# Kernel optimization log

Measured on AMD Instinct MI355X. Metric: run time of the kernel, lower is better.

The kernel has to match this reference:

```python
import jax, jax.numpy as jnp
import numpy as np

# ---- CRF hyperparameters (init_kwargs) ----
NUM_CLASSES = 4
RADIUS = 10            # guided filter radius -> 21x21 kernel
EPS = 1e-4
THETA_GAMMA = 2.5
G_RADIUS = int(THETA_GAMMA * 4)  # gaussian layer radius = 10 -> 21x21 kernel
SPATIAL_COMPAT = 3.0
BILATERAL_COMPAT = 10.0
NUM_ITERATIONS = 5
RGB_W = np.array([0.2989, 0.5870, 0.1140], dtype=np.float32)  # tf rgb_to_grayscale


def _make_kernel(radius, theta):
    x, y = np.mgrid[-radius:radius + 1, -radius:radius + 1]
    k = np.exp(-(x ** 2 + y ** 2) / (2.0 * theta ** 2))
    k = k / k.sum()
    k[radius, radius] = 0.0  # zero out center (no self-message)
    return jnp.asarray(k, dtype=jnp.float32)

_GAUSS_K = _make_kernel(G_RADIUS, THETA_GAMMA)          # spatial gaussian kernel
_GUIDED_K = _make_kernel(RADIUS, RADIUS / 3.0)          # guided-filter gaussian kernel


def _depthwise(src, k2d, r):
    # src: [B,H,W,C], k2d: [kh,kw]; zero-padded depthwise conv (same as pad+VALID)
    c = src.shape[-1]
    kh, kw = k2d.shape
    k = jnp.broadcast_to(k2d[:, :, None, None], (kh, kw, 1, c))
    return jax.lax.conv_general_dilated(
        src, k, window_strides=(1, 1), padding=[(r, r), (r, r)],
        dimension_numbers=('NHWC', 'HWIO', 'NHWC'), feature_group_count=c)


def _gaussian(src):
    return _depthwise(src, _GAUSS_K, G_RADIUS)


def _guided(gray, p):
    # guided gaussian filter with single-channel guide `gray` [B,H,W,1]
    gf = lambda s: _depthwise(s, _GUIDED_K, RADIUS)
    mean_I = gf(gray)                       # [B,H,W,1]
    mean_p = gf(p)                          # [B,H,W,C]
    mean_Ip = gf(gray * p)
    cov_Ip = mean_Ip - mean_I * mean_p
    mean_II = gf(gray * gray)
    var_I = mean_II - mean_I * mean_I
    a = cov_Ip / (var_I + EPS)
    b = mean_p - a * mean_I
    return gf(a) * gray + gf(b)


def setup_inputs() -> dict:
    key = jax.random.key(0)
    k1, k2 = jax.random.split(key)
    unary = jax.random.normal(k1, (1, 512, 512, NUM_CLASSES), dtype=jnp.float32)
    image = jax.random.uniform(k2, (1, 512, 512, 3), dtype=jnp.float32)
    return {"unary": unary, "image": image}


def reference(unary, image):
    gray = (image @ jnp.asarray(RGB_W))[..., None]        # [B,H,W,1]
    ones = jnp.ones_like(unary)
    spatial_norm = _gaussian(ones)
    bilateral_norm = _guided(gray, ones)

    Q = jax.nn.softmax(-unary, axis=-1)
    for _ in range(NUM_ITERATIONS):
        spatial_out = _gaussian(Q) / spatial_norm
        bilateral_out = _guided(gray, Q) / bilateral_norm
        # spatial_weights = SPATIAL_COMPAT*I, bilateral_weights = BILATERAL_COMPAT*I,
        # compatibility = -I  => matmuls reduce to scalar scaling + negation
        message = SPATIAL_COMPAT * spatial_out + BILATERAL_COMPAT * bilateral_out
        pairwise = -message
        Q = jax.nn.softmax(-unary - pairwise, axis=-1)
    return Q
```

## Files before the change

kernel.cpp:

```cpp
#include <hip/hip_runtime.h>
#include <hip/hip_cooperative_groups.h>
#include <hip/hip_fp16.h>
#include <math.h>

namespace cg = cooperative_groups;

#define W 512
#define H 512
#define NPIX (W*H)
#define RAD 10
#define KS 21
#define CRF_EPS 1e-4f

#define TX 32
#define TY 8
#define CIN (TX + 2*RAD)
#define RIN (TY + 2*RAD)
#define GX (W / TX)
#define GY (H / TY)
#define NBLK (GX*GY)
#define NVT (CIN * 4)

#define SM_BYTES 30784
#define SG_OFF 24960

struct W21 { float w[KS]; };

struct Params {
    const float4* unary;
    const float*  image;
    ushort4* Qh;
    float2*  a1b1;
    ushort4* ah;
    ushort4* bh;
    float4*  Qfinal;
    W21 wg, wu;
    float c0g, c0u;
};

__device__ __forceinline__ float4 f4(float x, float y, float z, float w_) {
    return make_float4(x, y, z, w_);
}
__device__ __forceinline__ float4 fma4(float s, float4 a, float4 acc) {
    acc.x = fmaf(s, a.x, acc.x); acc.y = fmaf(s, a.y, acc.y);
    acc.z = fmaf(s, a.z, acc.z); acc.w = fmaf(s, a.w, acc.w);
    return acc;
}
__device__ __forceinline__ int swz(int b, int N) {
    return (b & 7) * (N >> 3) + (b >> 3);
}
__device__ __forceinline__ ushort4 pack4(float4 v) {
    ushort4 r;
    r.x = __half_as_ushort(__float2half_rn(v.x));
    r.y = __half_as_ushort(__float2half_rn(v.y));
    r.z = __half_as_ushort(__float2half_rn(v.z));
    r.w = __half_as_ushort(__float2half_rn(v.w));
    return r;
}
__device__ __forceinline__ float4 unpack4(ushort4 v) {
    return f4(__half2float(__ushort_as_half(v.x)),
              __half2float(__ushort_as_half(v.y)),
              __half2float(__ushort_as_half(v.z)),
              __half2float(__ushort_as_half(v.w)));
}
__device__ __forceinline__ unsigned short packh(float v) {
    return __half_as_ushort(__float2half_rn(v));
}
__device__ __forceinline__ float unpackh(unsigned short v) {
    return __half2float(__ushort_as_half(v));
}


__global__ __launch_bounds__(256, 5) void k_crf(Params P) {
    cg::grid_group grid = cg::this_grid();
    __shared__ __align__(16) char smem[SM_BYTES];
    ushort4* sQh = (ushort4*)(smem + 13312);
    float4*  i0  = (float4*)smem;
    float4*  i1  = (float4*)(smem + 6656);
    float4*  i2  = (float4*)(smem + 13312);
    ushort4* sAB = (ushort4*)smem;
    float4*  ia  = (float4*)(smem + 11648);
    float4*  ib  = (float4*)(smem + 18304);
    float2*  s12 = (float2*)smem;
    float2*  ii1 = (float2*)(smem + 11648);
    float2*  ii0 = (float2*)smem;
    float*   sG  = (float*)(smem + SG_OFF);

    int t = threadIdx.x;
    int L = swz(blockIdx.x, NBLK);
    int x0 = (L & (GX - 1)) * TX, y0 = (L >> 4) * TY;
    int hrow = t >> 4, hx = (t & 15) * 2;
    int py = y0 + hrow, px0 = x0 + hx;
    int p0 = py * W + px0;
    int vc = t % CIN, vr0 = (t / CIN) * 2;
    int hbase = hrow * CIN + hx;
    int ccen = (hrow + RAD) * CIN + hx + RAD;

    {
        int pi = blockIdx.x * 256 + t;
        float4 u0 = P.unary[pi];
        float mn = fminf(fminf(u0.x, u0.y), fminf(u0.z, u0.w));
        float ex = expf(mn - u0.x), ey = expf(mn - u0.y);
        float ez = expf(mn - u0.z), ew = expf(mn - u0.w);
        float inv = 1.f / (ex + ey + ez + ew);
        P.Qh[pi] = pack4(f4(ex * inv, ey * inv, ez * inv, ew * inv));
    }
    for (int i = t; i < RIN * CIN; i += 256) {
        int r = i / CIN, c = i - r * CIN;
        int gx = x0 + c - RAD, gy = y0 + r - RAD;
        float g = 0.f;
        if ((unsigned)gx < W && (unsigned)gy < H) {
            int pp = gy * W + gx;
            g = 0.2989f * P.image[3 * pp] + 0.5870f * P.image[3 * pp + 1]
              + 0.1140f * P.image[3 * pp + 2];
        }
        sG[i] = g;
    }
    __syncthreads();
    float gc0 = 0.f, gc1 = 0.f, s3_0 = 0.f, s3_1 = 0.f;
    float Nu0 = 0.f, Nu1 = 0.f;
    if (t < 128) {
        gc0 = sG[ccen]; gc1 = sG[ccen + 1];
        float Sgx0 = 0.f, Sgx1 = 0.f, Sgy = 0.f;
        float Sux0 = 0.f, Sux1 = 0.f, Suy = 0.f;
        #pragma unroll
        for (int d = -RAD; d <= RAD; ++d) {
            int xa = px0 + d, xb = px0 + 1 + d, yy = py + d;
            float wgd = P.wg.w[d + RAD], wud = P.wu.w[d + RAD];
            if (xa >= 0 && xa < W) { Sgx0 += wgd; Sux0 += wud; }
            if (xb >= 0 && xb < W) { Sgx1 += wgd; Sux1 += wud; }
            if (yy >= 0 && yy < H) { Sgy  += wgd; Suy  += wud; }
        }
        s3_0 = 3.f / (Sgx0 * Sgy - P.c0g);
        s3_1 = 3.f / (Sgx1 * Sgy - P.c0g);
        Nu0 = Sux0 * Suy - P.c0u;
        Nu1 = Sux1 * Suy - P.c0u;
    }
    if (t < NVT) {
        float2 acc0 = make_float2(0.f, 0.f), acc1 = acc0;
        #pragma unroll
        for (int s = 0; s < 22; ++s) {
            float g = sG[(vr0 + s) * CIN + vc];
            if (s <= 20) { float wgv = P.wu.w[s] * g; acc0.x += wgv; acc0.y = fmaf(wgv, g, acc0.y); }
            if (s >= 1)  { float wgv = P.wu.w[s-1] * g; acc1.x += wgv; acc1.y = fmaf(wgv, g, acc1.y); }
        }
        ii0[vr0 * CIN + vc] = acc0;
        ii0[(vr0 + 1) * CIN + vc] = acc1;
    }
    __syncthreads();
    float mI0 = 0.f, mI1 = 0.f, iv0 = 0.f, iv1 = 0.f, ibn0 = 0.f, ibn1 = 0.f;
    if (t < 128) {
        float2 A0 = make_float2(0.f, 0.f), A1 = A0;
        #pragma unroll
        for (int d = 0; d < 22; ++d) {
            float2 v = ii0[hbase + d];
            if (d <= 20) { A0.x = fmaf(P.wu.w[d], v.x, A0.x); A0.y = fmaf(P.wu.w[d], v.y, A0.y); }
            if (d >= 1)  { A1.x = fmaf(P.wu.w[d-1], v.x, A1.x); A1.y = fmaf(P.wu.w[d-1], v.y, A1.y); }
        }
        mI0 = A0.x - P.c0u * gc0;
        float mII0 = A0.y - P.c0u * gc0 * gc0;
        iv0 = 1.f / ((mII0 - mI0 * mI0) + CRF_EPS);
        float a1v0 = mI0 * (1.f - Nu0) * iv0;
        P.a1b1[p0] = make_float2(a1v0, Nu0 - a1v0 * mI0);
        mI1 = A1.x - P.c0u * gc1;
        float mII1 = A1.y - P.c0u * gc1 * gc1;
        iv1 = 1.f / ((mII1 - mI1 * mI1) + CRF_EPS);
        float a1v1 = mI1 * (1.f - Nu1) * iv1;
        P.a1b1[p0 + 1] = make_float2(a1v1, Nu1 - a1v1 * mI1);
    }
    grid.sync();

    for (int i = t; i < RIN * CIN; i += 256) {
        int r = i / CIN, c = i - r * CIN;
        int gx = x0 + c - RAD, gy = y0 + r - RAD;
        float2 v = make_float2(0.f, 0.f);
        if ((unsigned)gx < W && (unsigned)gy < H) v = P.a1b1[gy * W + gx];
        s12[i] = v;
    }
    __syncthreads();
    if (t < NVT) {
        float2 acc0 = make_float2(0.f, 0.f), acc1 = acc0;
        #pragma unroll
        for (int s = 0; s < 22; ++s) {
            float2 v = s12[(vr0 + s) * CIN + vc];
            if (s <= 20) { acc0.x = fmaf(P.wu.w[s], v.x, acc0.x); acc0.y = fmaf(P.wu.w[s], v.y, acc0.y); }
            if (s >= 1)  { acc1.x = fmaf(P.wu.w[s-1], v.x, acc1.x); acc1.y = fmaf(P.wu.w[s-1], v.y, acc1.y); }
        }
        ii1[vr0 * CIN + vc] = acc0;
        ii1[(vr0 + 1) * CIN + vc] = acc1;
    }
    __syncthreads();
    if (t < 128) {
        float2 A0 = make_float2(0.f, 0.f), A1 = A0;
        #pragma unroll
        for (int d = 0; d < 22; ++d) {
            float2 v = ii1[hbase + d];
            if (d <= 20) { A0.x = fmaf(P.wu.w[d], v.x, A0.x); A0.y = fmaf(P.wu.w[d], v.y, A0.y); }
            if (d >= 1)  { A1.x = fmaf(P.wu.w[d-1], v.x, A1.x); A1.y = fmaf(P.wu.w[d-1], v.y, A1.y); }
        }
        float2 c0 = s12[ccen], c1 = s12[ccen + 1];
        ibn0 = 10.f / ((A0.x - P.c0u * c0.x) * gc0 + (A0.y - P.c0u * c0.y));
        ibn1 = 10.f / ((A1.x - P.c0u * c1.x) * gc1 + (A1.y - P.c0u * c1.y));
    }

    float4 part0, part1;
    for (int it = 0; it < 5; ++it) {
        __syncthreads();
        for (int i = t; i < RIN * CIN; i += 256) {
            int r = i / CIN, c = i - r * CIN;
            int gx = x0 + c - RAD, gy = y0 + r - RAD;
            ushort4 q = make_ushort4(0, 0, 0, 0);
            if ((unsigned)gx < W && (unsigned)gy < H) q = P.Qh[gy * W + gx];
            sQh[i] = q;
        }
        __syncthreads();
        float4 Qc0, Qc1;
        if (t < 128) { Qc0 = unpack4(sQh[ccen]); Qc1 = unpack4(sQh[ccen + 1]); }
        float4 a2h[2];
        if (t < NVT) {
            float4 a0[2], a1r[2];
            #pragma unroll
            for (int j = 0; j < 2; ++j) { a0[j] = f4(0,0,0,0); a1r[j] = a0[j]; a2h[j] = a0[j]; }
            #pragma unroll
            for (int s = 0; s < 22; ++s) {
                float4 q = unpack4(sQh[(vr0 + s) * CIN + vc]);
                float g = sG[(vr0 + s) * CIN + vc];
                float4 gq = f4(g * q.x, g * q.y, g * q.z, g * q.w);
                if (s <= 20) {
                    a0[0]  = fma4(P.wg.w[s], q, a0[0]);
                    a1r[0] = fma4(P.wu.w[s], q, a1r[0]);
                    a2h[0] = fma4(P.wu.w[s], gq, a2h[0]);
                }
                if (s >= 1) {
                    a0[1]  = fma4(P.wg.w[s-1], q, a0[1]);
                    a1r[1] = fma4(P.wu.w[s-1], q, a1r[1]);
                    a2h[1] = fma4(P.wu.w[s-1], gq, a2h[1]);
                }
            }
            i0[vr0 * CIN + vc] = a0[0];
            i0[(vr0 + 1) * CIN + vc] = a0[1];
            i1[vr0 * CIN + vc] = a1r[0];
            i1[(vr0 + 1) * CIN + vc] = a1r[1];
        }
        __syncthreads();
        if (t < NVT) {
            i2[vr0 * CIN + vc] = a2h[0];
            i2[(vr0 + 1) * CIN + vc] = a2h[1];
        }
        __syncthreads();
        if (t < 128) {
            float4 A0[2], A1[2], A2[2];
            #pragma unroll
            for (int j = 0; j < 2; ++j) { A0[j] = f4(0,0,0,0); A1[j] = A0[j]; A2[j] = A0[j]; }
            #pragma unroll
            for (int d = 0; d < 22; ++d) {
                float4 v0 = i0[hbase + d], v1 = i1[hbase + d], v2 = i2[hbase + d];
                if (d <= 20) {
                    A0[0] = fma4(P.wg.w[d], v0, A0[0]);
                    A1[0] = fma4(P.wu.w[d], v1, A1[0]);
                    A2[0] = fma4(P.wu.w[d], v2, A2[0]);
                }
                if (d >= 1) {
                    A0[1] = fma4(P.wg.w[d-1], v0, A0[1]);
                    A1[1] = fma4(P.wu.w[d-1], v1, A1[1]);
                    A2[1] = fma4(P.wu.w[d-1], v2, A2[1]);
                }
            }
            #pragma unroll
            for (int j = 0; j < 2; ++j) {
                float4 Qc = j ? Qc1 : Qc0;
                float gcj = j ? gc1 : gc0;
                float mIj = j ? mI1 : mI0, ivj = j ? iv1 : iv0;
                float s3j = j ? s3_1 : s3_0;
                float4 g4  = fma4(-P.c0g, Qc, A0[j]);
                float4 m4  = fma4(-P.c0u, Qc, A1[j]);
                float4 mi4 = fma4(-P.c0u * gcj, Qc, A2[j]);
                float4 a, b;
                a.x = (mi4.x - mIj * m4.x) * ivj; a.y = (mi4.y - mIj * m4.y) * ivj;
                a.z = (mi4.z - mIj * m4.z) * ivj; a.w = (mi4.w - mIj * m4.w) * ivj;
                b.x = m4.x - a.x * mIj; b.y = m4.y - a.y * mIj;
                b.z = m4.z - a.z * mIj; b.w = m4.w - a.w * mIj;
                float4 u = P.unary[p0 + j];
                float4 pt = f4(fmaf(s3j, g4.x, -u.x), fmaf(s3j, g4.y, -u.y),
                               fmaf(s3j, g4.z, -u.z), fmaf(s3j, g4.w, -u.w));
                if (j) part1 = pt; else part0 = pt;
                P.ah[p0 + j] = pack4(a); P.bh[p0 + j] = pack4(b);
            }
        }
        grid.sync();

        for (int i = t; i < RIN * CIN; i += 256) {
            int r = i / CIN, c = i - r * CIN;
            int gx = x0 + c - RAD, gy = y0 + r - RAD;
            ushort4 v = make_ushort4(0, 0, 0, 0);
            if ((unsigned)gx < W && (unsigned)gy < H) v = P.ah[gy * W + gx];
            sAB[i] = v;
        }
        __syncthreads();
        float4 Ac0, Ac1;
        if (t < 128) { Ac0 = unpack4(sAB[ccen]); Ac1 = unpack4(sAB[ccen + 1]); }
        if (t < NVT) {
            float4 va0 = f4(0,0,0,0), va1 = va0;
            #pragma unroll
            for (int s = 0; s < 22; ++s) {
                float4 v = unpack4(sAB[(vr0 + s) * CIN + vc]);
                if (s <= 20) va0 = fma4(P.wu.w[s], v, va0);
                if (s >= 1)  va1 = fma4(P.wu.w[s-1], v, va1);
            }
            ia[vr0 * CIN + vc] = va0;
            ia[(vr0 + 1) * CIN + vc] = va1;
        }
        __syncthreads();
        for (int i = t; i < RIN * CIN; i += 256) {
            int r = i / CIN, c = i - r * CIN;
            int gx = x0 + c - RAD, gy = y0 + r - RAD;
            ushort4 v = make_ushort4(0, 0, 0, 0);
            if ((unsigned)gx < W && (unsigned)gy < H) v = P.bh[gy * W + gx];
            sAB[i] = v;
        }
        __syncthreads();
        float4 Bc0, Bc1;
        if (t < 128) { Bc0 = unpack4(sAB[ccen]); Bc1 = unpack4(sAB[ccen + 1]); }
        if (t < NVT) {
            float4 vb0 = f4(0,0,0,0), vb1 = vb0;
            #pragma unroll
            for (int s = 0; s < 22; ++s) {
                float4 v = unpack4(sAB[(vr0 + s) * CIN + vc]);
                if (s <= 20) vb0 = fma4(P.wu.w[s], v, vb0);
                if (s >= 1)  vb1 = fma4(P.wu.w[s-1], v, vb1);
            }
            ib[vr0 * CIN + vc] = vb0;
            ib[(vr0 + 1) * CIN + vc] = vb1;
        }
        __syncthreads();
        if (t < 128) {
            float4 VA[2], VB[2];
            #pragma unroll
            for (int j = 0; j < 2; ++j) { VA[j] = f4(0,0,0,0); VB[j] = VA[j]; }
            #pragma unroll
            for (int d = 0; d < 22; ++d) {
                float4 va = ia[hbase + d], vb = ib[hbase + d];
                if (d <= 20) { VA[0] = fma4(P.wu.w[d], va, VA[0]); VB[0] = fma4(P.wu.w[d], vb, VB[0]); }
                if (d >= 1)  { VA[1] = fma4(P.wu.w[d-1], va, VA[1]); VB[1] = fma4(P.wu.w[d-1], vb, VB[1]); }
            }
            #pragma unroll
            for (int j = 0; j < 2; ++j) {
                float4 Ac = j ? Ac1 : Ac0, Bc = j ? Bc1 : Bc0;
                float gcj = j ? gc1 : gc0, ibnj = j ? ibn1 : ibn0;
                float4 pt = j ? part1 : part0;
                float4 a4 = fma4(-P.c0u, Ac, VA[j]);
                float4 b4 = fma4(-P.c0u, Bc, VB[j]);
                float lx = fmaf(fmaf(a4.x, gcj, b4.x), ibnj, pt.x);
                float ly = fmaf(fmaf(a4.y, gcj, b4.y), ibnj, pt.y);
                float lz = fmaf(fmaf(a4.z, gcj, b4.z), ibnj, pt.z);
                float lw = fmaf(fmaf(a4.w, gcj, b4.w), ibnj, pt.w);
                float m = fmaxf(fmaxf(lx, ly), fmaxf(lz, lw));
                float ex = expf(lx - m), ey = expf(ly - m);
                float ez = expf(lz - m), ew = expf(lw - m);
                float inv = 1.f / (ex + ey + ez + ew);
                float4 qn = f4(ex * inv, ey * inv, ez * inv, ew * inv);
                if (it == 4) P.Qfinal[p0 + j] = qn;
                else         P.Qh[p0 + j] = pack4(qn);
            }
        }
        if (it < 4) grid.sync();
    }
}


__global__ __launch_bounds__(256) void fb_init(const float* __restrict__ img,
        const float4* __restrict__ unary, unsigned short* __restrict__ grayh,
        ushort4* __restrict__ Qh, float* __restrict__ Sg, float* __restrict__ Su,
        W21 wg, W21 wu) {
    int t = threadIdx.x;
    if (blockIdx.x < 2) {
        int x = blockIdx.x * 256 + t;
        float sg = 0.f, su = 0.f;
        #pragma unroll
        for (int d = -RAD; d <= RAD; ++d) {
            int xx = x + d;
            if (xx >= 0 && xx < W) { sg += wg.w[d + RAD]; su += wu.w[d + RAD]; }
        }
        Sg[x] = sg; Su[x] = su;
    }
    int b = swz(blockIdx.x, NPIX / 256);
    int p = b * 256 + t;
    float r = img[3 * p], g = img[3 * p + 1], bch = img[3 * p + 2];
    grayh[p] = packh(0.2989f * r + 0.5870f * g + 0.1140f * bch);
    float4 u = unary[p];
    float mn = fminf(fminf(u.x, u.y), fminf(u.z, u.w));
    float ex = expf(mn - u.x), ey = expf(mn - u.y), ez = expf(mn - u.z), ew = expf(mn - u.w);
    float inv = 1.f / (ex + ey + ez + ew);
    Qh[p] = pack4(f4(ex * inv, ey * inv, ez * inv, ew * inv));
}

__global__ __launch_bounds__(256, 4) void fb_s1(const unsigned short* __restrict__ grayh,
        const float* __restrict__ Su, float* __restrict__ mean_I,
        float* __restrict__ inv_var, float2* __restrict__ a1b1,
        W21 wu, float c0u) {
    __shared__ float  sg[RIN][CIN];
    __shared__ float2 ii[TY][CIN];
    int L = swz(blockIdx.x, NBLK);
    int x0 = (L & (GX - 1)) * TX, y0 = (L >> 4) * TY;
    int t = threadIdx.x;
    for (int i = t; i < RIN * CIN; i += 256) {
        int r = i / CIN, c = i - r * CIN;
        int gx = x0 + c - RAD, gy = y0 + r - RAD;
        float g = 0.f;
        if ((unsigned)gx < W && (unsigned)gy < H) g = unpackh(grayh[gy * W + gx]);
        sg[r][c] = g;
    }
    __syncthreads();
    if (t < NVT) {
        int c = t % CIN, r0 = (t / CIN) * 2;
        float2 acc0 = make_float2(0.f, 0.f), acc1 = acc0;
        #pragma unroll
        for (int s = 0; s < 22; ++s) {
            float g = sg[r0 + s][c];
            if (s <= 20) { float wgv = wu.w[s] * g; acc0.x += wgv; acc0.y = fmaf(wgv, g, acc0.y); }
            if (s >= 1)  { float wgv = wu.w[s-1] * g; acc1.x += wgv; acc1.y = fmaf(wgv, g, acc1.y); }
        }
        ii[r0][c] = acc0; ii[r0 + 1][c] = acc1;
    }
    __syncthreads();
    int row = t >> 5, col = t & 31;
    float2 A = make_float2(0.f, 0.f);
    #pragma unroll
    for (int d = 0; d < KS; ++d) {
        float2 v = ii[row][col + d];
        A.x = fmaf(wu.w[d], v.x, A.x);
        A.y = fmaf(wu.w[d], v.y, A.y);
    }
    int py = y0 + row, px = x0 + col;
    int p = py * W + px;
    float gc = sg[row + RAD][col + RAD];
    float mI = A.x - c0u * gc;
    float mII = A.y - c0u * gc * gc;
    float iv = 1.f / ((mII - mI * mI) + CRF_EPS);
    float N = Su[px] * Su[py] - c0u;
    float av = mI * (1.f - N) * iv;
    float bv = N - av * mI;
    mean_I[p] = mI; inv_var[p] = iv; a1b1[p] = make_float2(av, bv);
}

__global__ __launch_bounds__(256, 4) void fb_s2(const float2* __restrict__ a1b1,
        const unsigned short* __restrict__ grayh, float* __restrict__ inv_bn,
        W21 wu, float c0u) {
    __shared__ float2 s2[RIN][CIN];
    __shared__ float2 ii[TY][CIN];
    int L = swz(blockIdx.x, NBLK);
    int x0 = (L & (GX - 1)) * TX, y0 = (L >> 4) * TY;
    int t = threadIdx.x;
    for (int i = t; i < RIN * CIN; i += 256) {
        int r = i / CIN, c = i - r * CIN;
        int gx = x0 + c - RAD, gy = y0 + r - RAD;
        float2 v = make_float2(0.f, 0.f);
        if ((unsigned)gx < W && (unsigned)gy < H) v = a1b1[gy * W + gx];
        s2[r][c] = v;
    }
    __syncthreads();
    if (t < NVT) {
        int c = t % CIN, r0 = (t / CIN) * 2;
        float2 acc0 = make_float2(0.f, 0.f), acc1 = acc0;
        #pragma unroll
        for (int s = 0; s < 22; ++s) {
            float2 v = s2[r0 + s][c];
            if (s <= 20) { acc0.x = fmaf(wu.w[s], v.x, acc0.x); acc0.y = fmaf(wu.w[s], v.y, acc0.y); }
            if (s >= 1)  { acc1.x = fmaf(wu.w[s-1], v.x, acc1.x); acc1.y = fmaf(wu.w[s-1], v.y, acc1.y); }
        }
        ii[r0][c] = acc0; ii[r0 + 1][c] = acc1;
    }
    __syncthreads();
    int row = t >> 5, col = t & 31;
    float2 A = make_float2(0.f, 0.f);
    #pragma unroll
    for (int d = 0; d < KS; ++d) {
        float2 v = ii[row][col + d];
        A.x = fmaf(wu.w[d], v.x, A.x);
        A.y = fmaf(wu.w[d], v.y, A.y);
    }
    int p = (y0 + row) * W + x0 + col;
    float2 cen = s2[row + RAD][col + RAD];
    float va = A.x - c0u * cen.x;
    float vb = A.y - c0u * cen.y;
    inv_bn[p] = 1.f / (va * unpackh(grayh[p]) + vb);
}

__global__ __launch_bounds__(256, 4) void fb_f1(const ushort4* __restrict__ Qh,
        const unsigned short* __restrict__ grayh, const float* __restrict__ mean_I,
        const float* __restrict__ inv_var, const float* __restrict__ Sg,
        const float4* __restrict__ unary, ushort4* __restrict__ a_out,
        ushort4* __restrict__ b_out, float4* __restrict__ partial,
        W21 wg, W21 wu, float c0g, float c0u) {
    __shared__ __align__(16) char smem[23296 + 5824 + 6656];
    float4* sQ = (float4*)smem;
    float*  sG = (float*)(smem + 23296);
    float4* i2 = (float4*)(smem + 23296 + 5824);
    float4* i0 = (float4*)smem;
    float4* i1 = (float4*)(smem + 6656);
    int L = swz(blockIdx.x, NBLK);
    int x0 = (L & (GX - 1)) * TX, y0 = (L >> 4) * TY;
    int t = threadIdx.x;
    for (int i = t; i < RIN * CIN; i += 256) {
        int r = i / CIN, c = i - r * CIN;
        int gx = x0 + c - RAD, gy = y0 + r - RAD;
        float4 q = f4(0.f, 0.f, 0.f, 0.f); float g = 0.f;
        if ((unsigned)gx < W && (unsigned)gy < H) {
            int p = gy * W + gx; q = unpack4(Qh[p]); g = unpackh(grayh[p]);
        }
        sQ[i] = q; sG[i] = g;
    }
    __syncthreads();
    int row = t >> 5, col = t & 31;
    int py = y0 + row, px = x0 + col;
    int p = py * W + px;
    float mI = mean_I[p], iv = inv_var[p];
    float4 u = unary[p];
    float sgx = Sg[px], sgy = Sg[py];
    float4 Qc = sQ[(row + RAD) * CIN + col + RAD];
    float  gc = sG[(row + RAD) * CIN + col + RAD];
    float4 a0[2], a1[2], a2[2];
    int vc = t % CIN, vr0 = (t / CIN) * 2;
    if (t < NVT) {
        #pragma unroll
        for (int j = 0; j < 2; ++j) { a0[j] = f4(0,0,0,0); a1[j] = a0[j]; a2[j] = a0[j]; }
        #pragma unroll
        for (int s = 0; s < 22; ++s) {
            float4 q = sQ[(vr0 + s) * CIN + vc];
            float g = sG[(vr0 + s) * CIN + vc];
            float4 gq = f4(g * q.x, g * q.y, g * q.z, g * q.w);
            if (s <= 20) {
                a0[0] = fma4(wg.w[s], q, a0[0]);
                a1[0] = fma4(wu.w[s], q, a1[0]);
                a2[0] = fma4(wu.w[s], gq, a2[0]);
            }
            if (s >= 1) {
                a0[1] = fma4(wg.w[s-1], q, a0[1]);
                a1[1] = fma4(wu.w[s-1], q, a1[1]);
                a2[1] = fma4(wu.w[s-1], gq, a2[1]);
            }
        }
    }
    __syncthreads();
    if (t < NVT) {
        #pragma unroll
        for (int j = 0; j < 2; ++j) {
            i0[(vr0 + j) * CIN + vc] = a0[j];
            i1[(vr0 + j) * CIN + vc] = a1[j];
            i2[(vr0 + j) * CIN + vc] = a2[j];
        }
    }
    __syncthreads();
    float4 A0 = f4(0,0,0,0), A1 = A0, A2 = A0;
    #pragma unroll
    for (int d = 0; d < KS; ++d) {
        A0 = fma4(wg.w[d], i0[row * CIN + col + d], A0);
        A1 = fma4(wu.w[d], i1[row * CIN + col + d], A1);
        A2 = fma4(wu.w[d], i2[row * CIN + col + d], A2);
    }
    float4 g4  = fma4(-c0g, Qc, A0);
    float4 m4  = fma4(-c0u, Qc, A1);
    float4 mi4 = fma4(-c0u * gc, Qc, A2);
    float4 a, b;
    a.x = (mi4.x - mI * m4.x) * iv; a.y = (mi4.y - mI * m4.y) * iv;
    a.z = (mi4.z - mI * m4.z) * iv; a.w = (mi4.w - mI * m4.w) * iv;
    b.x = m4.x - a.x * mI; b.y = m4.y - a.y * mI;
    b.z = m4.z - a.z * mI; b.w = m4.w - a.w * mI;
    float s3 = 3.f / (sgx * sgy - c0g);
    float4 part = f4(fmaf(s3, g4.x, -u.x), fmaf(s3, g4.y, -u.y),
                     fmaf(s3, g4.z, -u.z), fmaf(s3, g4.w, -u.w));
    a_out[p] = pack4(a); b_out[p] = pack4(b); partial[p] = part;
}

__global__ __launch_bounds__(256, 4) void fb_f2(const ushort4* __restrict__ A,
        const ushort4* __restrict__ B, const float4* __restrict__ partial,
        const unsigned short* __restrict__ grayh, const float* __restrict__ inv_bn,
        float4* __restrict__ QoutF, ushort4* __restrict__ QoutH, int last,
        W21 wu, float c0u) {
    __shared__ __align__(16) char smem[23296 + 6656];
    float4* sT = (float4*)smem;
    float4* ia = (float4*)(smem + 23296);
    float4* ib = (float4*)smem;
    int L = swz(blockIdx.x, NBLK);
    int x0 = (L & (GX - 1)) * TX, y0 = (L >> 4) * TY;
    int t = threadIdx.x;
    int row = t >> 5, col = t & 31;
    int py = y0 + row, px = x0 + col;
    int p = py * W + px;
    int vc = t % CIN, vr0 = (t / CIN) * 2;
    float gv = unpackh(grayh[p]);
    float ibn = 10.f * inv_bn[p];
    float4 part = partial[p];
    for (int i = t; i < RIN * CIN; i += 256) {
        int r = i / CIN, c = i - r * CIN;
        int gx = x0 + c - RAD, gy = y0 + r - RAD;
        float4 v = f4(0.f, 0.f, 0.f, 0.f);
        if ((unsigned)gx < W && (unsigned)gy < H) v = unpack4(A[gy * W + gx]);
        sT[i] = v;
    }
    __syncthreads();
    float4 Ac = sT[(row + RAD) * CIN + col + RAD];
    float4 va0 = f4(0,0,0,0), va1 = va0;
    if (t < NVT) {
        #pragma unroll
        for (int s = 0; s < 22; ++s) {
            float4 v = sT[(vr0 + s) * CIN + vc];
            if (s <= 20) va0 = fma4(wu.w[s], v, va0);
            if (s >= 1)  va1 = fma4(wu.w[s-1], v, va1);
        }
        ia[vr0 * CIN + vc] = va0;
        ia[(vr0 + 1) * CIN + vc] = va1;
    }
    __syncthreads();
    for (int i = t; i < RIN * CIN; i += 256) {
        int r = i / CIN, c = i - r * CIN;
        int gx = x0 + c - RAD, gy = y0 + r - RAD;
        float4 v = f4(0.f, 0.f, 0.f, 0.f);
        if ((unsigned)gx < W && (unsigned)gy < H) v = unpack4(B[gy * W + gx]);
        sT[i] = v;
    }
    __syncthreads();
    float4 Bc = sT[(row + RAD) * CIN + col + RAD];
    float4 vb0 = f4(0,0,0,0), vb1 = vb0;
    if (t < NVT) {
        #pragma unroll
        for (int s = 0; s < 22; ++s) {
            float4 v = sT[(vr0 + s) * CIN + vc];
            if (s <= 20) vb0 = fma4(wu.w[s], v, vb0);
            if (s >= 1)  vb1 = fma4(wu.w[s-1], v, vb1);
        }
    }
    __syncthreads();
    if (t < NVT) {
        ib[vr0 * CIN + vc] = vb0;
        ib[(vr0 + 1) * CIN + vc] = vb1;
    }
    __syncthreads();
    float4 VA = f4(0,0,0,0), VB = VA;
    #pragma unroll
    for (int d = 0; d < KS; ++d) {
        VA = fma4(wu.w[d], ia[row * CIN + col + d], VA);
        VB = fma4(wu.w[d], ib[row * CIN + col + d], VB);
    }
    float4 a4 = fma4(-c0u, Ac, VA);
    float4 b4 = fma4(-c0u, Bc, VB);
    float lx = fmaf(fmaf(a4.x, gv, b4.x), ibn, part.x);
    float ly = fmaf(fmaf(a4.y, gv, b4.y), ibn, part.y);
    float lz = fmaf(fmaf(a4.z, gv, b4.z), ibn, part.z);
    float lw = fmaf(fmaf(a4.w, gv, b4.w), ibn, part.w);
    float m = fmaxf(fmaxf(lx, ly), fmaxf(lz, lw));
    float ex = expf(lx - m), ey = expf(ly - m), ez = expf(lz - m), ew = expf(lw - m);
    float inv = 1.f / (ex + ey + ez + ew);
    float4 qn = f4(ex * inv, ey * inv, ez * inv, ew * inv);
    if (last) QoutF[p] = qn;
    else      QoutH[p] = pack4(qn);
}


static void make_w_host(double theta, W21* w, float* c0) {
    double tmp[KS], s = 0.0;
    for (int d = -RAD; d <= RAD; ++d) {
        double v = exp(-(double)(d * d) / (2.0 * theta * theta));
        tmp[d + RAD] = v; s += v;
    }
    for (int i = 0; i < KS; ++i) w->w[i] = (float)(tmp[i] / s);
    *c0 = (float)(1.0 / (s * s));
}

extern "C" void kernel_launch(void* const* d_in, const int* in_sizes, int n_in,
                              void* d_out, int out_size, void* d_ws, size_t ws_size,
                              hipStream_t stream) {
    const float4* unary = (const float4*)d_in[0];
    const float* image = (const float*)d_in[1];
    char* wsb = (char*)d_ws;

    unsigned short* grayh = (unsigned short*)wsb;
    ushort4* Qh      = (ushort4*)(wsb + 524288);
    ushort4* ah      = (ushort4*)(wsb + 2621440);
    ushort4* bh      = (ushort4*)(wsb + 4718592);
    float4*  partial = (float4*)(wsb + 6815744);
    float*   mean_I  = (float*)(wsb + 11010048);
    float*   inv_var = (float*)(wsb + 12058624);
    float*   inv_bn  = (float*)(wsb + 13107200);
    float2*  a1b1    = (float2*)(wsb + 14155776);
    float*   Sg      = (float*)(wsb + 16252928);
    float*   Su      = (float*)(wsb + 16255040);

    W21 wg, wu; float c0g, c0u;
    make_w_host(2.5, &wg, &c0g);
    make_w_host(10.0 / 3.0, &wu, &c0u);

    int dev = 0;
    (void)hipGetDevice(&dev);
    int coop = 0, nCU = 0, blkPerCU = 0;
    (void)hipDeviceGetAttribute(&coop, hipDeviceAttributeCooperativeLaunch, dev);
    (void)hipDeviceGetAttribute(&nCU, hipDeviceAttributeMultiprocessorCount, dev);
    (void)hipOccupancyMaxActiveBlocksPerMultiprocessor(&blkPerCU,
            (const void*)k_crf, 256, 0);
    bool useCoop = (coop != 0) && ((long)blkPerCU * nCU >= NBLK);

    hipError_t st = hipErrorUnknown;
    if (useCoop) {
        Params P;
        P.unary = unary; P.image = image; P.Qh = Qh;
        P.a1b1 = a1b1; P.ah = ah; P.bh = bh;
        P.Qfinal = (float4*)d_out;
        P.wg = wg; P.wu = wu; P.c0g = c0g; P.c0u = c0u;
        void* args[] = { &P };
        st = hipLaunchCooperativeKernel((const void*)k_crf, dim3(NBLK), dim3(256),
                                        args, 0, stream);
    }
    if (st != hipSuccess) {
        dim3 bl(256), grEl(NPIX / 256), grT(NBLK);
        fb_init<<<grEl, bl, 0, stream>>>(image, unary, grayh, Qh, Sg, Su, wg, wu);
        fb_s1<<<grT, bl, 0, stream>>>(grayh, Su, mean_I, inv_var, a1b1, wu, c0u);
        fb_s2<<<grT, bl, 0, stream>>>(a1b1, grayh, inv_bn, wu, c0u);
        for (int it = 0; it < 5; ++it) {
            fb_f1<<<grT, bl, 0, stream>>>(Qh, grayh, mean_I, inv_var, Sg,
                                          unary, ah, bh, partial, wg, wu, c0g, c0u);
            fb_f2<<<grT, bl, 0, stream>>>(ah, bh, partial, grayh, inv_bn,
                                          (float4*)d_out, Qh, (it == 4) ? 1 : 0,
                                          wu, c0u);
        }
    }
}
```

Measured before the change: 171.7 us.

## Store fp16 gray globally, pad LDS rows, and hoist unary loads

Computes grayscale once per pixel into a global fp16 buffer, at the cost of an extra grid sync before the halo tiles are loaded. Each iteration now reloads gray from that buffer alongside Q instead of keeping a persistent fp32 gray tile in LDS. Intermediate row buffers use a padded stride (53) to reduce LDS bank conflicts, and unary values are held in registers instead of being reloaded each iteration. The shared memory layout is reorganized, which raises LDS use slightly and may affect occupancy; gray is stored in fp16 for all iterations, which lowers its precision.

```diff
diff --git a/kernel.cpp b/kernel.cpp
--- a/kernel.cpp
+++ b/kernel.cpp
@@ -15,20 +15,24 @@
 #define TX 32
 #define TY 8
 #define CIN (TX + 2*RAD)
+#define CINP 53
 #define RIN (TY + 2*RAD)
 #define GX (W / TX)
 #define GY (H / TY)
 #define NBLK (GX*GY)
 #define NVT (CIN * 4)
 
-#define SM_BYTES 30784
-#define SG_OFF 24960
+#define OFF_I0 11648
+#define OFF_I1 18432
+#define OFF_SLOTC 25216
+#define SM_BYTES 32000
 
 struct W21 { float w[KS]; };
 
 struct Params {
     const float4* unary;
     const float*  image;
+    unsigned short* grayh;
     ushort4* Qh;
     float2*  a1b1;
     ushort4* ah;
@@ -74,17 +78,17 @@
 __global__ __launch_bounds__(256, 5) void k_crf(Params P) {
     cg::grid_group grid = cg::this_grid();
     __shared__ __align__(16) char smem[SM_BYTES];
-    ushort4* sQh = (ushort4*)(smem + 13312);
-    float4*  i0  = (float4*)smem;
-    float4*  i1  = (float4*)(smem + 6656);
-    float4*  i2  = (float4*)(smem + 13312);
-    ushort4* sAB = (ushort4*)smem;
-    float4*  ia  = (float4*)(smem + 11648);
-    float4*  ib  = (float4*)(smem + 18304);
-    float2*  s12 = (float2*)smem;
-    float2*  ii1 = (float2*)(smem + 11648);
-    float2*  ii0 = (float2*)smem;
-    float*   sG  = (float*)(smem + SG_OFF);
+    ushort4* tile = (ushort4*)smem;
+    float4*  i0   = (float4*)(smem + OFF_I0);
+    float4*  i1   = (float4*)(smem + OFF_I1);
+    float4*  i2   = (float4*)(smem + OFF_SLOTC);
+    unsigned short* sGh = (unsigned short*)(smem + OFF_SLOTC);
+    float4*  ia   = (float4*)(smem + OFF_I0);
+    float4*  ib   = (float4*)(smem + OFF_I1);
+    float*   sGf  = (float*)smem;
+    float2*  ii0  = (float2*)(smem + 5824);
+    float2*  s12  = (float2*)smem;
+    float2*  ii1  = (float2*)(smem + 11648);
 
     int t = threadIdx.x;
     int L = swz(blockIdx.x, NBLK);
@@ -93,11 +97,13 @@
     int py = y0 + hrow, px0 = x0 + hx;
     int p0 = py * W + px0;
     int vc = t % CIN, vr0 = (t / CIN) * 2;
-    int hbase = hrow * CIN + hx;
+    int hb = hrow * CINP + hx;
     int ccen = (hrow + RAD) * CIN + hx + RAD;
 
     {
         int pi = blockIdx.x * 256 + t;
+        float r = P.image[3 * pi], g = P.image[3 * pi + 1], b = P.image[3 * pi + 2];
+        P.grayh[pi] = packh(0.2989f * r + 0.5870f * g + 0.1140f * b);
         float4 u0 = P.unary[pi];
         float mn = fminf(fminf(u0.x, u0.y), fminf(u0.z, u0.w));
         float ex = expf(mn - u0.x), ey = expf(mn - u0.y);
@@ -105,22 +111,11 @@
         float inv = 1.f / (ex + ey + ez + ew);
         P.Qh[pi] = pack4(f4(ex * inv, ey * inv, ez * inv, ew * inv));
     }
-    for (int i = t; i < RIN * CIN; i += 256) {
-        int r = i / CIN, c = i - r * CIN;
-        int gx = x0 + c - RAD, gy = y0 + r - RAD;
-        float g = 0.f;
-        if ((unsigned)gx < W && (unsigned)gy < H) {
-            int pp = gy * W + gx;
-            g = 0.2989f * P.image[3 * pp] + 0.5870f * P.image[3 * pp + 1]
-              + 0.1140f * P.image[3 * pp + 2];
-        }
-        sG[i] = g;
-    }
-    __syncthreads();
-    float gc0 = 0.f, gc1 = 0.f, s3_0 = 0.f, s3_1 = 0.f;
-    float Nu0 = 0.f, Nu1 = 0.f;
+    float4 u[2]; float s3[2], Nu[2];
+    float gcp[2], mIp[2], ivp[2], ibnp[2];
+    float4 partp[2];
     if (t < 128) {
-        gc0 = sG[ccen]; gc1 = sG[ccen + 1];
+        u[0] = P.unary[p0]; u[1] = P.unary[p0 + 1];
         float Sgx0 = 0.f, Sgx1 = 0.f, Sgy = 0.f;
         float Sux0 = 0.f, Sux1 = 0.f, Suy = 0.f;
         #pragma unroll
@@ -131,42 +126,53 @@
             if (xb >= 0 && xb < W) { Sgx1 += wgd; Sux1 += wud; }
             if (yy >= 0 && yy < H) { Sgy  += wgd; Suy  += wud; }
         }
-        s3_0 = 3.f / (Sgx0 * Sgy - P.c0g);
-        s3_1 = 3.f / (Sgx1 * Sgy - P.c0g);
-        Nu0 = Sux0 * Suy - P.c0u;
-        Nu1 = Sux1 * Suy - P.c0u;
-    }
-    if (t < NVT) {
-        float2 acc0 = make_float2(0.f, 0.f), acc1 = acc0;
+        s3[0] = 3.f / (Sgx0 * Sgy - P.c0g);
+        s3[1] = 3.f / (Sgx1 * Sgy - P.c0g);
+        Nu[0] = Sux0 * Suy - P.c0u;
+        Nu[1] = Sux1 * Suy - P.c0u;
+    }
+    grid.sync();
+
+    for (int i = t; i < RIN * CIN; i += 256) {
+        int r = i / CIN, c = i - r * CIN;
+        int gx = x0 + c - RAD, gy = y0 + r - RAD;
+        float g = 0.f;
+        if ((unsigned)gx < W && (unsigned)gy < H) g = unpackh(P.grayh[gy * W + gx]);
+        sGf[i] = g;
+    }
+    __syncthreads();
+    if (t < NVT) {
+        float2 a0 = make_float2(0.f, 0.f), a1 = a0;
         #pragma unroll
         for (int s = 0; s < 22; ++s) {
-            float g = sG[(vr0 + s) * CIN + vc];
-            if (s <= 20) { float wgv = P.wu.w[s] * g; acc0.x += wgv; acc0.y = fmaf(wgv, g, acc0.y); }
-            if (s >= 1)  { float wgv = P.wu.w[s-1] * g; acc1.x += wgv; acc1.y = fmaf(wgv, g, acc1.y); }
-        }
-        ii0[vr0 * CIN + vc] = acc0;
-        ii0[(vr0 + 1) * CIN + vc] = acc1;
-    }
-    __syncthreads();
-    float mI0 = 0.f, mI1 = 0.f, iv0 = 0.f, iv1 = 0.f, ibn0 = 0.f, ibn1 = 0.f;
+            float g = sGf[(vr0 + s) * CIN + vc];
+            if (s <= 20) { float wv = P.wu.w[s] * g; a0.x += wv; a0.y = fmaf(wv, g, a0.y); }
+            if (s >= 1)  { float wv = P.wu.w[s-1] * g; a1.x += wv; a1.y = fmaf(wv, g, a1.y); }
+        }
+        ii0[vr0 * CINP + vc] = a0;
+        ii0[(vr0 + 1) * CINP + vc] = a1;
+    }
+    __syncthreads();
     if (t < 128) {
         float2 A0 = make_float2(0.f, 0.f), A1 = A0;
         #pragma unroll
         for (int d = 0; d < 22; ++d) {
-            float2 v = ii0[hbase + d];
+            float2 v = ii0[hb + d];
             if (d <= 20) { A0.x = fmaf(P.wu.w[d], v.x, A0.x); A0.y = fmaf(P.wu.w[d], v.y, A0.y); }
             if (d >= 1)  { A1.x = fmaf(P.wu.w[d-1], v.x, A1.x); A1.y = fmaf(P.wu.w[d-1], v.y, A1.y); }
         }
-        mI0 = A0.x - P.c0u * gc0;
-        float mII0 = A0.y - P.c0u * gc0 * gc0;
-        iv0 = 1.f / ((mII0 - mI0 * mI0) + CRF_EPS);
-        float a1v0 = mI0 * (1.f - Nu0) * iv0;
-        P.a1b1[p0] = make_float2(a1v0, Nu0 - a1v0 * mI0);
-        mI1 = A1.x - P.c0u * gc1;
-        float mII1 = A1.y - P.c0u * gc1 * gc1;
-        iv1 = 1.f / ((mII1 - mI1 * mI1) + CRF_EPS);
-        float a1v1 = mI1 * (1.f - Nu1) * iv1;
-        P.a1b1[p0 + 1] = make_float2(a1v1, Nu1 - a1v1 * mI1);
+        gcp[0] = sGf[ccen]; gcp[1] = sGf[ccen + 1];
+        #pragma unroll
+        for (int j = 0; j < 2; ++j) {
+            float2 A = j ? A1 : A0;
+            float gc = gcp[j];
+            float mI = A.x - P.c0u * gc;
+            float mII = A.y - P.c0u * gc * gc;
+            float iv = 1.f / ((mII - mI * mI) + CRF_EPS);
+            float a1v = mI * (1.f - Nu[j]) * iv;
+            P.a1b1[p0 + j] = make_float2(a1v, Nu[j] - a1v * mI);
+            mIp[j] = mI; ivp[j] = iv;
+        }
     }
     grid.sync();
 
@@ -179,43 +185,49 @@
     }
     __syncthreads();
     if (t < NVT) {
-        float2 acc0 = make_float2(0.f, 0.f), acc1 = acc0;
+        float2 a0 = make_float2(0.f, 0.f), a1 = a0;
         #pragma unroll
         for (int s = 0; s < 22; ++s) {
             float2 v = s12[(vr0 + s) * CIN + vc];
-            if (s <= 20) { acc0.x = fmaf(P.wu.w[s], v.x, acc0.x); acc0.y = fmaf(P.wu.w[s], v.y, acc0.y); }
-            if (s >= 1)  { acc1.x = fmaf(P.wu.w[s-1], v.x, acc1.x); acc1.y = fmaf(P.wu.w[s-1], v.y, acc1.y); }
-        }
-        ii1[vr0 * CIN + vc] = acc0;
-        ii1[(vr0 + 1) * CIN + vc] = acc1;
+            if (s <= 20) { a0.x = fmaf(P.wu.w[s], v.x, a0.x); a0.y = fmaf(P.wu.w[s], v.y, a0.y); }
+            if (s >= 1)  { a1.x = fmaf(P.wu.w[s-1], v.x, a1.x); a1.y = fmaf(P.wu.w[s-1], v.y, a1.y); }
+        }
+        ii1[vr0 * CINP + vc] = a0;
+        ii1[(vr0 + 1) * CINP + vc] = a1;
     }
     __syncthreads();
     if (t < 128) {
         float2 A0 = make_float2(0.f, 0.f), A1 = A0;
         #pragma unroll
         for (int d = 0; d < 22; ++d) {
-            float2 v = ii1[hbase + d];
+            float2 v = ii1[hb + d];
             if (d <= 20) { A0.x = fmaf(P.wu.w[d], v.x, A0.x); A0.y = fmaf(P.wu.w[d], v.y, A0.y); }
             if (d >= 1)  { A1.x = fmaf(P.wu.w[d-1], v.x, A1.x); A1.y = fmaf(P.wu.w[d-1], v.y, A1.y); }
         }
-        float2 c0 = s12[ccen], c1 = s12[ccen + 1];
-        ibn0 = 10.f / ((A0.x - P.c0u * c0.x) * gc0 + (A0.y - P.c0u * c0.y));
-        ibn1 = 10.f / ((A1.x - P.c0u * c1.x) * gc1 + (A1.y - P.c0u * c1.y));
-    }
-
-    float4 part0, part1;
+        #pragma unroll
+        for (int j = 0; j < 2; ++j) {
+            float2 A = j ? A1 : A0;
+            float2 cen = s12[ccen + j];
+            float va = A.x - P.c0u * cen.x;
+            float vb = A.y - P.c0u * cen.y;
+            ibnp[j] = 10.f / (va * gcp[j] + vb);
+        }
+    }
+
     for (int it = 0; it < 5; ++it) {
         __syncthreads();
         for (int i = t; i < RIN * CIN; i += 256) {
             int r = i / CIN, c = i - r * CIN;
             int gx = x0 + c - RAD, gy = y0 + r - RAD;
-            ushort4 q = make_ushort4(0, 0, 0, 0);
-            if ((unsigned)gx < W && (unsigned)gy < H) q = P.Qh[gy * W + gx];
-            sQh[i] = q;
+            ushort4 q = make_ushort4(0, 0, 0, 0); unsigned short g = 0;
+            if ((unsigned)gx < W && (unsigned)gy < H) {
+                int pp = gy * W + gx; q = P.Qh[pp]; g = P.grayh[pp];
+            }
+            tile[i] = q; sGh[i] = g;
         }
         __syncthreads();
-        float4 Qc0, Qc1;
-        if (t < 128) { Qc0 = unpack4(sQh[ccen]); Qc1 = unpack4(sQh[ccen + 1]); }
+        float4 Qc[2];
+        if (t < 128) { Qc[0] = unpack4(tile[ccen]); Qc[1] = unpack4(tile[ccen + 1]); }
         float4 a2h[2];
         if (t < NVT) {
             float4 a0[2], a1r[2];
@@ -223,8 +235,8 @@
             for (int j = 0; j < 2; ++j) { a0[j] = f4(0,0,0,0); a1r[j] = a0[j]; a2h[j] = a0[j]; }
             #pragma unroll
             for (int s = 0; s < 22; ++s) {
-                float4 q = unpack4(sQh[(vr0 + s) * CIN + vc]);
-                float g = sG[(vr0 + s) * CIN + vc];
+                float4 q = unpack4(tile[(vr0 + s) * CIN + vc]);
+                float g = unpackh(sGh[(vr0 + s) * CIN + vc]);
                 float4 gq = f4(g * q.x, g * q.y, g * q.z, g * q.w);
                 if (s <= 20) {
                     a0[0]  = fma4(P.wg.w[s], q, a0[0]);
@@ -237,15 +249,15 @@
                     a2h[1] = fma4(P.wu.w[s-1], gq, a2h[1]);
                 }
             }
-            i0[vr0 * CIN + vc] = a0[0];
-            i0[(vr0 + 1) * CIN + vc] = a0[1];
-            i1[vr0 * CIN + vc] = a1r[0];
-            i1[(vr0 + 1) * CIN + vc] = a1r[1];
+            i0[vr0 * CINP + vc] = a0[0];
+            i0[(vr0 + 1) * CINP + vc] = a0[1];
+            i1[vr0 * CINP + vc] = a1r[0];
+            i1[(vr0 + 1) * CINP + vc] = a1r[1];
         }
         __syncthreads();
         if (t < NVT) {
-            i2[vr0 * CIN + vc] = a2h[0];
-            i2[(vr0 + 1) * CIN + vc] = a2h[1];
+            i2[vr0 * CINP + vc] = a2h[0];
+            i2[(vr0 + 1) * CINP + vc] = a2h[1];
         }
         __syncthreads();
         if (t < 128) {
@@ -254,7 +266,7 @@
             for (int j = 0; j < 2; ++j) { A0[j] = f4(0,0,0,0); A1[j] = A0[j]; A2[j] = A0[j]; }
             #pragma unroll
             for (int d = 0; d < 22; ++d) {
-                float4 v0 = i0[hbase + d], v1 = i1[hbase + d], v2 = i2[hbase + d];
+                float4 v0 = i0[hb + d], v1 = i1[hb + d], v2 = i2[hb + d];
                 if (d <= 20) {
                     A0[0] = fma4(P.wg.w[d], v0, A0[0]);
                     A1[0] = fma4(P.wu.w[d], v1, A1[0]);
@@ -268,22 +280,17 @@
             }
             #pragma unroll
             for (int j = 0; j < 2; ++j) {
-                float4 Qc = j ? Qc1 : Qc0;
-                float gcj = j ? gc1 : gc0;
-                float mIj = j ? mI1 : mI0, ivj = j ? iv1 : iv0;
-                float s3j = j ? s3_1 : s3_0;
-                float4 g4  = fma4(-P.c0g, Qc, A0[j]);
-                float4 m4  = fma4(-P.c0u, Qc, A1[j]);
-                float4 mi4 = fma4(-P.c0u * gcj, Qc, A2[j]);
+                float4 g4  = fma4(-P.c0g, Qc[j], A0[j]);
+                float4 m4  = fma4(-P.c0u, Qc[j], A1[j]);
+                float4 mi4 = fma4(-P.c0u * gcp[j], Qc[j], A2[j]);
+                float mI = mIp[j], iv = ivp[j];
                 float4 a, b;
-                a.x = (mi4.x - mIj * m4.x) * ivj; a.y = (mi4.y - mIj * m4.y) * ivj;
-                a.z = (mi4.z - mIj * m4.z) * ivj; a.w = (mi4.w - mIj * m4.w) * ivj;
-                b.x = m4.x - a.x * mIj; b.y = m4.y - a.y * mIj;
-                b.z = m4.z - a.z * mIj; b.w = m4.w - a.w * mIj;
-                float4 u = P.unary[p0 + j];
-                float4 pt = f4(fmaf(s3j, g4.x, -u.x), fmaf(s3j, g4.y, -u.y),
-                               fmaf(s3j, g4.z, -u.z), fmaf(s3j, g4.w, -u.w));
-                if (j) part1 = pt; else part0 = pt;
+                a.x = (mi4.x - mI * m4.x) * iv; a.y = (mi4.y - mI * m4.y) * iv;
+                a.z = (mi4.z - mI * m4.z) * iv; a.w = (mi4.w - mI * m4.w) * iv;
+                b.x = m4.x - a.x * mI; b.y = m4.y - a.y * mI;
+                b.z = m4.z - a.z * mI; b.w = m4.w - a.w * mI;
+                partp[j] = f4(fmaf(s3[j], g4.x, -u[j].x), fmaf(s3[j], g4.y, -u[j].y),
+                              fmaf(s3[j], g4.z, -u[j].z), fmaf(s3[j], g4.w, -u[j].w));
                 P.ah[p0 + j] = pack4(a); P.bh[p0 + j] = pack4(b);
             }
         }
@@ -294,21 +301,21 @@
             int gx = x0 + c - RAD, gy = y0 + r - RAD;
             ushort4 v = make_ushort4(0, 0, 0, 0);
             if ((unsigned)gx < W && (unsigned)gy < H) v = P.ah[gy * W + gx];
-            sAB[i] = v;
+            tile[i] = v;
         }
         __syncthreads();
-        float4 Ac0, Ac1;
-        if (t < 128) { Ac0 = unpack4(sAB[ccen]); Ac1 = unpack4(sAB[ccen + 1]); }
+        float4 Ac[2];
+        if (t < 128) { Ac[0] = unpack4(tile[ccen]); Ac[1] = unpack4(tile[ccen + 1]); }
         if (t < NVT) {
             float4 va0 = f4(0,0,0,0), va1 = va0;
             #pragma unroll
             for (int s = 0; s < 22; ++s) {
-                float4 v = unpack4(sAB[(vr0 + s) * CIN + vc]);
+                float4 v = unpack4(tile[(vr0 + s) * CIN + vc]);
                 if (s <= 20) va0 = fma4(P.wu.w[s], v, va0);
                 if (s >= 1)  va1 = fma4(P.wu.w[s-1], v, va1);
             }
-            ia[vr0 * CIN + vc] = va0;
-            ia[(vr0 + 1) * CIN + vc] = va1;
+            ia[vr0 * CINP + vc] = va0;
+            ia[(vr0 + 1) * CINP + vc] = va1;
         }
         __syncthreads();
         for (int i = t; i < RIN * CIN; i += 256) {
@@ -316,21 +323,21 @@
             int gx = x0 + c - RAD, gy = y0 + r - RAD;
             ushort4 v = make_ushort4(0, 0, 0, 0);
             if ((unsigned)gx < W && (unsigned)gy < H) v = P.bh[gy * W + gx];
-            sAB[i] = v;
+            tile[i] = v;
         }
         __syncthreads();
-        float4 Bc0, Bc1;
-        if (t < 128) { Bc0 = unpack4(sAB[ccen]); Bc1 = unpack4(sAB[ccen + 1]); }
+        float4 Bc[2];
+        if (t < 128) { Bc[0] = unpack4(tile[ccen]); Bc[1] = unpack4(tile[ccen + 1]); }
         if (t < NVT) {
             float4 vb0 = f4(0,0,0,0), vb1 = vb0;
             #pragma unroll
             for (int s = 0; s < 22; ++s) {
-                float4 v = unpack4(sAB[(vr0 + s) * CIN + vc]);
+                float4 v = unpack4(tile[(vr0 + s) * CIN + vc]);
                 if (s <= 20) vb0 = fma4(P.wu.w[s], v, vb0);
                 if (s >= 1)  vb1 = fma4(P.wu.w[s-1], v, vb1);
             }
-            ib[vr0 * CIN + vc] = vb0;
-            ib[(vr0 + 1) * CIN + vc] = vb1;
+            ib[vr0 * CINP + vc] = vb0;
+            ib[(vr0 + 1) * CINP + vc] = vb1;
         }
         __syncthreads();
         if (t < 128) {
@@ -339,21 +346,20 @@
             for (int j = 0; j < 2; ++j) { VA[j] = f4(0,0,0,0); VB[j] = VA[j]; }
             #pragma unroll
             for (int d = 0; d < 22; ++d) {
-                float4 va = ia[hbase + d], vb = ib[hbase + d];
+                float4 va = ia[hb + d], vb = ib[hb + d];
                 if (d <= 20) { VA[0] = fma4(P.wu.w[d], va, VA[0]); VB[0] = fma4(P.wu.w[d], vb, VB[0]); }
                 if (d >= 1)  { VA[1] = fma4(P.wu.w[d-1], va, VA[1]); VB[1] = fma4(P.wu.w[d-1], vb, VB[1]); }
             }
             #pragma unroll
             for (int j = 0; j < 2; ++j) {
-                float4 Ac = j ? Ac1 : Ac0, Bc = j ? Bc1 : Bc0;
-                float gcj = j ? gc1 : gc0, ibnj = j ? ibn1 : ibn0;
-                float4 pt = j ? part1 : part0;
-                float4 a4 = fma4(-P.c0u, Ac, VA[j]);
-                float4 b4 = fma4(-P.c0u, Bc, VB[j]);
-                float lx = fmaf(fmaf(a4.x, gcj, b4.x), ibnj, pt.x);
-                float ly = fmaf(fmaf(a4.y, gcj, b4.y), ibnj, pt.y);
-                float lz = fmaf(fmaf(a4.z, gcj, b4.z), ibnj, pt.z);
-                float lw = fmaf(fmaf(a4.w, gcj, b4.w), ibnj, pt.w);
+                float4 a4 = fma4(-P.c0u, Ac[j], VA[j]);
+                float4 b4 = fma4(-P.c0u, Bc[j], VB[j]);
+                float gc = gcp[j], ibn = ibnp[j];
+                float4 pt = partp[j];
+                float lx = fmaf(fmaf(a4.x, gc, b4.x), ibn, pt.x);
+                float ly = fmaf(fmaf(a4.y, gc, b4.y), ibn, pt.y);
+                float lz = fmaf(fmaf(a4.z, gc, b4.z), ibn, pt.z);
+                float lw = fmaf(fmaf(a4.w, gc, b4.w), ibn, pt.w);
                 float m = fmaxf(fmaxf(lx, ly), fmaxf(lz, lw));
                 float ex = expf(lx - m), ey = expf(ly - m);
                 float ez = expf(lz - m), ew = expf(lw - m);
@@ -702,7 +708,7 @@
     hipError_t st = hipErrorUnknown;
     if (useCoop) {
         Params P;
-        P.unary = unary; P.image = image; P.Qh = Qh;
+        P.unary = unary; P.image = image; P.grayh = grayh; P.Qh = Qh;
         P.a1b1 = a1b1; P.ah = ah; P.bh = bh;
         P.Qfinal = (float4*)d_out;
         P.wg = wg; P.wu = wu; P.c0g = c0g; P.c0u = c0u;
```

Measured after the change: 170.7 us. About the same (-0.6%).
